# Performance work log

Measured on AMD Instinct MI355X. Metric: run time of the kernel, lower is better.

Reference implementation:

```python
import jax, jax.numpy as jnp
import numpy as np

D_MODEL = 1024
NHEAD = 16
HEAD_DIM = D_MODEL // NHEAD


def setup_inputs() -> dict:
    key = jax.random.key(0)
    ks = jax.random.split(key, 11)
    B, S = 2, 2048
    s = 1.0 / np.sqrt(D_MODEL)
    return {
        "query": jax.random.normal(ks[0], (B, S, D_MODEL), jnp.float32),
        "key": jax.random.normal(ks[1], (B, S, D_MODEL), jnp.float32),
        "value": jax.random.normal(ks[2], (B, S, D_MODEL), jnp.float32),
        "wq_w": jax.random.normal(ks[3], (D_MODEL, D_MODEL), jnp.float32) * s,
        "wq_b": jax.random.normal(ks[4], (D_MODEL,), jnp.float32) * s,
        "wk_w": jax.random.normal(ks[5], (D_MODEL, D_MODEL), jnp.float32) * s,
        "wk_b": jax.random.normal(ks[6], (D_MODEL,), jnp.float32) * s,
        "wv_w": jax.random.normal(ks[7], (D_MODEL, D_MODEL), jnp.float32) * s,
        "wv_b": jax.random.normal(ks[8], (D_MODEL,), jnp.float32) * s,
        "wo_w": jax.random.normal(ks[9], (D_MODEL, D_MODEL), jnp.float32) * s,
        "wo_b": jax.random.normal(ks[10], (D_MODEL,), jnp.float32) * s,
    }


def reference(query, key, value, wq_w, wq_b, wk_w, wk_b, wv_w, wv_b, wo_w, wo_b):
    B, S, _ = query.shape
    # torch Linear: x @ W.T + b
    def proj(x, w, b):
        y = x @ w.T + b
        return y.reshape(B, S, NHEAD, HEAD_DIM).transpose(0, 2, 1, 3)  # [B,H,S,Dh]

    Q = proj(query, wq_w, wq_b)
    K = proj(key, wk_w, wk_b)
    V = proj(value, wv_w, wv_b)

    scale = 1.0 / np.sqrt(HEAD_DIM).astype(np.float32)
    scores = jnp.einsum("bhqd,bhkd->bhqk", Q, K) * scale  # [B,H,S,S]
    causal = jnp.tril(jnp.ones((S, S), dtype=bool))
    scores = jnp.where(causal, scores, -jnp.inf)
    attn = jax.nn.softmax(scores, axis=-1)
    out = jnp.einsum("bhqk,bhkd->bhqd", attn, V)  # [B,H,S,Dh]
    out = out.transpose(0, 2, 1, 3).reshape(B, S, D_MODEL)
    return out @ wo_w.T + wo_b
```

## Files before the change

kernel.cpp:

```cpp
#include <hip/hip_runtime.h>
#include <stdint.h>

#define D_MODEL 1024
#define S_LEN   2048
#define NHEAD   16
#define HEAD_DIM 64
#define BATCH   2
#define M_TOT   (BATCH * S_LEN)
#define Q_SCALE 0.18033688011112042f

using bf16x8 = __attribute__((ext_vector_type(8))) short;
using f32x4  = __attribute__((ext_vector_type(4))) float;

__device__ __forceinline__ unsigned short f2bf(float f) {
  union { float f; unsigned int u; } v; v.f = f;
  unsigned int u = v.u;
  return (unsigned short)((u + 0x7FFFu + ((u >> 16) & 1u)) >> 16);
}
__device__ __forceinline__ unsigned int pkbf(float a, float b) {
#if __has_builtin(__builtin_amdgcn_cvt_pk_bf16_f32)
  auto p = __builtin_amdgcn_cvt_pk_bf16_f32(a, b);
  union { decltype(p) v; unsigned int u; } c; c.v = p;
  return c.u;
#else
  return (unsigned int)f2bf(a) | ((unsigned int)f2bf(b) << 16);
#endif
}
__device__ __forceinline__ bf16x8 cvt8(const float* p) {
  const float4 a = *(const float4*)p;
  const float4 b = *(const float4*)(p + 4);
  union { unsigned int u[4]; bf16x8 v; } r;
  r.u[0] = pkbf(a.x, a.y); r.u[1] = pkbf(a.z, a.w);
  r.u[2] = pkbf(b.x, b.y); r.u[3] = pkbf(b.z, b.w);
  return r.v;
}
__device__ __forceinline__ float fexp2(float x) {
#if __has_builtin(__builtin_amdgcn_exp2f)
  return __builtin_amdgcn_exp2f(x);
#else
  return __expf(x * 0.69314718055994531f);
#endif
}
__device__ __forceinline__ void async16(const unsigned short* g, short* l) {
  __builtin_amdgcn_global_load_lds(
      reinterpret_cast<const __attribute__((address_space(1))) unsigned int*>(
          reinterpret_cast<uintptr_t>(g)),
      reinterpret_cast<__attribute__((address_space(3))) unsigned int*>(
          reinterpret_cast<uintptr_t>(l)),
      16, 0, 0);
}

__device__ __forceinline__ void swap32(unsigned int& x, unsigned int& y) {
#if __has_builtin(__builtin_amdgcn_permlane32_swap)
  auto r = __builtin_amdgcn_permlane32_swap(x, y, false, false);
  x = (unsigned int)r[0]; y = (unsigned int)r[1];
#else
  const int lane = threadIdx.x & 63;
  unsigned int sx = (unsigned int)__shfl_xor((int)x, 32);
  unsigned int sy = (unsigned int)__shfl_xor((int)y, 32);
  unsigned int nx = (lane & 32) ? sy : x;
  unsigned int ny = (lane & 32) ? y : sx;
  x = nx; y = ny;
#endif
}
__device__ __forceinline__ void swap16(unsigned int& x, unsigned int& y) {
#if __has_builtin(__builtin_amdgcn_permlane16_swap)
  auto r = __builtin_amdgcn_permlane16_swap(x, y, false, false);
  x = (unsigned int)r[0]; y = (unsigned int)r[1];
#else
  const int lane = threadIdx.x & 63;
  unsigned int sx = (unsigned int)__shfl_xor((int)x, 16);
  unsigned int sy = (unsigned int)__shfl_xor((int)y, 16);
  unsigned int nx = (lane & 16) ? sy : x;
  unsigned int ny = (lane & 16) ? y : sx;
  x = nx; y = ny;
#endif
}

#define LDK 40

__global__ __launch_bounds__(256)
void cast_all(const float* __restrict__ wq, const float* __restrict__ wk,
              const float* __restrict__ wv, const float* __restrict__ wo,
              const float* __restrict__ q, const float* __restrict__ k,
              const float* __restrict__ v,
              unsigned short* __restrict__ wb,
              unsigned short* __restrict__ qb, unsigned short* __restrict__ kb,
              unsigned short* __restrict__ vb)
{
  const int z = blockIdx.y;
  const float* src;
  unsigned short* d;
  size_t n;
  switch (z) {
    case 0: src = wq; d = wb;                                   n = (size_t)D_MODEL * D_MODEL; break;
    case 1: src = wk; d = wb + (size_t)1 * D_MODEL * D_MODEL;   n = (size_t)D_MODEL * D_MODEL; break;
    case 2: src = wv; d = wb + (size_t)2 * D_MODEL * D_MODEL;   n = (size_t)D_MODEL * D_MODEL; break;
    case 3: src = wo; d = wb + (size_t)3 * D_MODEL * D_MODEL;   n = (size_t)D_MODEL * D_MODEL; break;
    case 4: src = q;  d = qb;                                   n = (size_t)M_TOT * D_MODEL;   break;
    case 5: src = k;  d = kb;                                   n = (size_t)M_TOT * D_MODEL;   break;
    default: src = v; d = vb;                                   n = (size_t)M_TOT * D_MODEL;   break;
  }
  const size_t i = ((size_t)blockIdx.x * 256 + threadIdx.x) * 8;
  if (i < n) *(bf16x8*)(d + i) = cvt8(src + i);
}

__device__ __forceinline__ void gemm_tile_lds(const unsigned short* __restrict__ A,
                                              const unsigned short* __restrict__ W,
                                              int m0, int n0,
                                              short* As, short* Bs,
                                              f32x4 acc[4][4])
{
  const int t    = threadIdx.x;
  const int lane = t & 63;
  const int w    = t >> 6;
  const int quad = lane >> 4;
  const int l16  = lane & 15;
  const int wm   = (w >> 1) * 64;
  const int wn   = (w & 1) * 64;
  const int srow = w * 16 + (lane >> 2);
  const int scol = (lane & 3) * 8;

  for (int mt = 0; mt < 4; ++mt)
    for (int nt = 0; nt < 4; ++nt)
      acc[mt][nt] = f32x4{0.f, 0.f, 0.f, 0.f};

  for (int kt = 0; kt < D_MODEL / 32; ++kt) {
    const int kc = kt * 32 + scol;
    __syncthreads();
    async16(A + (size_t)(m0 + srow)      * D_MODEL + kc, As + srow * 32 + scol);
    async16(A + (size_t)(m0 + 64 + srow) * D_MODEL + kc, As + (64 + srow) * 32 + scol);
    async16(W + (size_t)(n0 + srow)      * D_MODEL + kc, Bs + srow * 32 + scol);
    async16(W + (size_t)(n0 + 64 + srow) * D_MODEL + kc, Bs + (64 + srow) * 32 + scol);
    __syncthreads();

    bf16x8 af[4], bfr[4];
    for (int mt = 0; mt < 4; ++mt)
      af[mt] = *(const bf16x8*)(As + (wm + mt * 16 + l16) * 32 + quad * 8);
    for (int nt = 0; nt < 4; ++nt)
      bfr[nt] = *(const bf16x8*)(Bs + (wn + nt * 16 + l16) * 32 + quad * 8);
    for (int mt = 0; mt < 4; ++mt)
      for (int nt = 0; nt < 4; ++nt)
        acc[mt][nt] = __builtin_amdgcn_mfma_f32_16x16x32_bf16(af[mt], bfr[nt], acc[mt][nt], 0, 0, 0);
  }
}

__device__ __forceinline__ void gemm_tile_f32(const float* __restrict__ A,
                                              const unsigned short* __restrict__ W,
                                              int m0, int n0,
                                              short* As, short* Bs,
                                              f32x4 acc[4][4])
{
  const int t    = threadIdx.x;
  const int lane = t & 63;
  const int w    = t >> 6;
  const int quad = lane >> 4;
  const int l16  = lane & 15;
  const int wm   = (w >> 1) * 64;
  const int wn   = (w & 1) * 64;
  const int srow = t >> 2;
  const int scol = (t & 3) * 8;

  for (int mt = 0; mt < 4; ++mt)
    for (int nt = 0; nt < 4; ++nt)
      acc[mt][nt] = f32x4{0.f, 0.f, 0.f, 0.f};

  for (int kt = 0; kt < D_MODEL / 32; ++kt) {
    const int kc = kt * 32 + scol;
    const bf16x8 a0 = cvt8(A + (size_t)(m0 + srow)      * D_MODEL + kc);
    const bf16x8 a1 = cvt8(A + (size_t)(m0 + srow + 64) * D_MODEL + kc);
    const bf16x8 b0 = *(const bf16x8*)(W + (size_t)(n0 + srow)      * D_MODEL + kc);
    const bf16x8 b1 = *(const bf16x8*)(W + (size_t)(n0 + srow + 64) * D_MODEL + kc);
    __syncthreads();
    *(bf16x8*)(As + (srow)      * LDK + scol) = a0;
    *(bf16x8*)(As + (srow + 64) * LDK + scol) = a1;
    *(bf16x8*)(Bs + (srow)      * LDK + scol) = b0;
    *(bf16x8*)(Bs + (srow + 64) * LDK + scol) = b1;
    __syncthreads();

    bf16x8 af[4], bfr[4];
    for (int mt = 0; mt < 4; ++mt)
      af[mt] = *(const bf16x8*)(As + (wm + mt * 16 + l16) * LDK + quad * 8);
    for (int nt = 0; nt < 4; ++nt)
      bfr[nt] = *(const bf16x8*)(Bs + (wn + nt * 16 + l16) * LDK + quad * 8);
    for (int mt = 0; mt < 4; ++mt)
      for (int nt = 0; nt < 4; ++nt)
        acc[mt][nt] = __builtin_amdgcn_mfma_f32_16x16x32_bf16(af[mt], bfr[nt], acc[mt][nt], 0, 0, 0);
  }
}

__device__ __forceinline__ void qkv_epilogue(int z, int m0, int n0,
                                             const float* __restrict__ bias,
                                             float scale,
                                             unsigned short* __restrict__ dst,
                                             f32x4 acc[4][4])
{
  const int t    = threadIdx.x;
  const int lane = t & 63;
  const int w    = t >> 6;
  const int quad = lane >> 4;
  const int l16  = lane & 15;
  const int wm   = (w >> 1) * 64;
  const int wn   = (w & 1) * 64;

  for (int nt = 0; nt < 4; ++nt) {
    const int n = n0 + wn + nt * 16 + l16;
    const float bb = bias[n];
    const int h = n >> 6, d = n & 63;
    for (int mt = 0; mt < 4; ++mt) {
      for (int r = 0; r < 4; ++r) {
        const int m = m0 + wm + mt * 16 + quad * 4 + r;
        const int b = m >> 11, s = m & 2047;
        const unsigned short val = f2bf((acc[mt][nt][r] + bb) * scale);
        if (z < 2)
          dst[((size_t)((b * NHEAD + h) * S_LEN + s)) * HEAD_DIM + d] = val;
        else
          dst[((size_t)((b * NHEAD + h) * HEAD_DIM + d)) * S_LEN + s] = val;
      }
    }
  }
}

__global__ __launch_bounds__(256)
void qkv_fast(const unsigned short* __restrict__ qb,
              const unsigned short* __restrict__ kb,
              const unsigned short* __restrict__ vb,
              const unsigned short* __restrict__ wqb,
              const unsigned short* __restrict__ wkb,
              const unsigned short* __restrict__ wvb,
              const float* __restrict__ bq, const float* __restrict__ bk,
              const float* __restrict__ bv,
              unsigned short* __restrict__ Qh, unsigned short* __restrict__ Kh,
              unsigned short* __restrict__ VhT)
{
  __shared__ __attribute__((aligned(16))) short As[128 * 32];
  __shared__ __attribute__((aligned(16))) short Bs[128 * 32];
  const int z = blockIdx.z;
  const unsigned short* A    = (z == 0) ? qb  : (z == 1) ? kb  : vb;
  const unsigned short* W    = (z == 0) ? wqb : (z == 1) ? wkb : wvb;
  const float*          bias = (z == 0) ? bq  : (z == 1) ? bk  : bv;
  unsigned short*       dst  = (z == 0) ? Qh  : (z == 1) ? Kh  : VhT;
  const float           scale = (z == 0) ? Q_SCALE : 1.0f;

  const int m0 = blockIdx.x * 128, n0 = blockIdx.y * 128;
  f32x4 acc[4][4];
  gemm_tile_lds(A, W, m0, n0, As, Bs, acc);
  qkv_epilogue(z, m0, n0, bias, scale, dst, acc);
}

__global__ __launch_bounds__(256)
void qkv_slow(const float* __restrict__ query, const float* __restrict__ key,
              const float* __restrict__ value,
              const unsigned short* __restrict__ wqb,
              const unsigned short* __restrict__ wkb,
              const unsigned short* __restrict__ wvb,
              const float* __restrict__ bq, const float* __restrict__ bk,
              const float* __restrict__ bv,
              unsigned short* __restrict__ Qh, unsigned short* __restrict__ Kh,
              unsigned short* __restrict__ VhT)
{
  __shared__ __attribute__((aligned(16))) short As[128 * LDK];
  __shared__ __attribute__((aligned(16))) short Bs[128 * LDK];
  const int z = blockIdx.z;
  const float*          A    = (z == 0) ? query : (z == 1) ? key : value;
  const unsigned short* W    = (z == 0) ? wqb   : (z == 1) ? wkb : wvb;
  const float*          bias = (z == 0) ? bq    : (z == 1) ? bk  : bv;
  unsigned short*       dst  = (z == 0) ? Qh    : (z == 1) ? Kh  : VhT;
  const float           scale = (z == 0) ? Q_SCALE : 1.0f;

  const int m0 = blockIdx.x * 128, n0 = blockIdx.y * 128;
  f32x4 acc[4][4];
  gemm_tile_f32(A, W, m0, n0, As, Bs, acc);
  qkv_epilogue(z, m0, n0, bias, scale, dst, acc);
}

__global__ __launch_bounds__(256)
void out_proj(const unsigned short* __restrict__ Oh,
              const unsigned short* __restrict__ wob,
              const float* __restrict__ bo,
              float* __restrict__ dst)
{
  __shared__ __attribute__((aligned(16))) short As[128 * 32];
  __shared__ __attribute__((aligned(16))) short Bs[128 * 32];
  const int m0 = blockIdx.x * 128, n0 = blockIdx.y * 128;
  f32x4 acc[4][4];
  gemm_tile_lds(Oh, wob, bo ? m0 : m0, n0, As, Bs, acc);

  const int t    = threadIdx.x;
  const int lane = t & 63;
  const int w    = t >> 6;
  const int quad = lane >> 4;
  const int l16  = lane & 15;
  const int wm   = (w >> 1) * 64;
  const int wn   = (w & 1) * 64;

  for (int nt = 0; nt < 4; ++nt) {
    const int n = n0 + wn + nt * 16 + l16;
    const float bb = bo[n];
    for (int mt = 0; mt < 4; ++mt)
      for (int r = 0; r < 4; ++r) {
        const int m = m0 + wm + mt * 16 + quad * 4 + r;
        dst[(size_t)m * D_MODEL + n] = acc[mt][nt][r] + bb;
      }
  }
}

__global__ __launch_bounds__(256)
void attn_kernel(const unsigned short* __restrict__ Qh,
                 const unsigned short* __restrict__ Kh,
                 const unsigned short* __restrict__ VhT,
                 unsigned short* __restrict__ O)
{
  __shared__ __attribute__((aligned(16))) short Ks[128 * 72];
  __shared__ __attribute__((aligned(16))) short Vts[64 * 136];

  const int bh   = blockIdx.x;
  const int qt   = (int)gridDim.y - 1 - (int)blockIdx.y;
  const int q0   = qt * 64;
  const int b    = bh >> 4;
  const int h    = bh & 15;
  const int t    = threadIdx.x;
  const int w    = t >> 6;
  const int lane = t & 63;
  const int quad = lane >> 4;
  const int l16  = lane & 15;
  const size_t headK = (size_t)bh * S_LEN * HEAD_DIM;
  const size_t headV = (size_t)bh * HEAD_DIM * S_LEN;

  bf16x8 qf[2];
  {
    const size_t qrow = (size_t)bh * S_LEN + (q0 + w * 16 + l16);
    qf[0] = *(const bf16x8*)(Qh + qrow * HEAD_DIM + quad * 8);
    qf[1] = *(const bf16x8*)(Qh + qrow * HEAD_DIM + 32 + quad * 8);
  }
  bf16x8 ones;
  for (int j = 0; j < 8; ++j) ones[j] = (short)0x3F80;

  f32x4 lacc = f32x4{0.f, 0.f, 0.f, 0.f};
  f32x4 oacc[4];
  for (int dt = 0; dt < 4; ++dt) oacc[dt] = f32x4{0.f, 0.f, 0.f, 0.f};

  const int rowbase = q0 + w * 16;
  const int rowmax  = rowbase + 15;
  const int qg      = rowbase + l16;
  const int kr = t >> 3, kc = (t & 7) * 8;
  const int vd = t >> 4, vc = (t & 15) * 8;

  const int nkt = (qt + 2) >> 1;
  for (int kt = 0; kt < nkt; ++kt) {
    const int k0 = kt * 128;
    __syncthreads();
    for (int i = 0; i < 4; ++i) {
      const int rr = kr + i * 32;
      *(bf16x8*)(Ks + rr * 72 + kc) =
          *(const bf16x8*)(Kh + headK + (size_t)(k0 + rr) * HEAD_DIM + kc);
      const int dd = vd + i * 16;
      *(bf16x8*)(Vts + dd * 136 + vc) =
          *(const bf16x8*)(VhT + headV + (size_t)dd * S_LEN + k0 + vc);
    }
    __syncthreads();

    float st[8][4];
#pragma unroll
    for (int nt = 0; nt < 8; ++nt) {
      const int c0 = k0 + nt * 16;
      if (c0 <= rowmax) {
        f32x4 s = f32x4{0.f, 0.f, 0.f, 0.f};
#pragma unroll
        for (int ks = 0; ks < 2; ++ks) {
          const bf16x8 kf = *(const bf16x8*)(Ks + (nt * 16 + l16) * 72 + ks * 32 + quad * 8);
          s = __builtin_amdgcn_mfma_f32_16x16x32_bf16(kf, qf[ks], s, 0, 0, 0);
        }
        if (c0 + 15 <= rowbase) {
#pragma unroll
          for (int r = 0; r < 4; ++r) st[nt][r] = fexp2(s[r]);
        } else {
          const int kgb = c0 + quad * 4;
#pragma unroll
          for (int r = 0; r < 4; ++r)
            st[nt][r] = (kgb + r <= qg) ? fexp2(s[r]) : 0.f;
        }
      } else {
#pragma unroll
        for (int r = 0; r < 4; ++r) st[nt][r] = 0.f;
      }
    }

#pragma unroll
    for (int ks = 0; ks < 4; ++ks) {
      if (k0 + ks * 32 <= rowmax) {
        unsigned int pa = pkbf(st[2 * ks][0],     st[2 * ks][1]);
        unsigned int pb = pkbf(st[2 * ks][2],     st[2 * ks][3]);
        unsigned int pc = pkbf(st[2 * ks + 1][0], st[2 * ks + 1][1]);
        unsigned int pe = pkbf(st[2 * ks + 1][2], st[2 * ks + 1][3]);
        swap32(pa, pc); swap32(pb, pe);
        swap16(pa, pc); swap16(pb, pe);
        union { unsigned int u[4]; bf16x8 v; } pf;
        pf.u[0] = pa; pf.u[1] = pb; pf.u[2] = pc; pf.u[3] = pe;
        lacc = __builtin_amdgcn_mfma_f32_16x16x32_bf16(pf.v, ones, lacc, 0, 0, 0);
#pragma unroll
        for (int dt = 0; dt < 4; ++dt) {
          const bf16x8 vf = *(const bf16x8*)(Vts + (dt * 16 + l16) * 136 + ks * 32 + quad * 8);
          oacc[dt] = __builtin_amdgcn_mfma_f32_16x16x32_bf16(pf.v, vf, oacc[dt], 0, 0, 0);
        }
      }
    }
  }

  for (int dt = 0; dt < 4; ++dt) {
    for (int r = 0; r < 4; ++r) {
      const int rowg = q0 + w * 16 + quad * 4 + r;
      O[(size_t)(b * S_LEN + rowg) * D_MODEL + h * 64 + dt * 16 + l16] =
          f2bf(oacc[dt][r] / lacc[r]);
    }
  }
}

extern "C" void kernel_launch(void* const* d_in, const int* in_sizes, int n_in,
                              void* d_out, int out_size, void* d_ws, size_t ws_size,
                              hipStream_t stream)
{
  (void)in_sizes; (void)n_in; (void)out_size;
  const float* q  = (const float*)d_in[0];
  const float* k  = (const float*)d_in[1];
  const float* v  = (const float*)d_in[2];
  const float* wq = (const float*)d_in[3];
  const float* bq = (const float*)d_in[4];
  const float* wk = (const float*)d_in[5];
  const float* bk = (const float*)d_in[6];
  const float* wv = (const float*)d_in[7];
  const float* bv = (const float*)d_in[8];
  const float* wo = (const float*)d_in[9];
  const float* bo = (const float*)d_in[10];
  float* out = (float*)d_out;

  unsigned short* wb  = (unsigned short*)d_ws;
  unsigned short* wqb = wb;
  unsigned short* wkb = wb + (size_t)1 * D_MODEL * D_MODEL;
  unsigned short* wvb = wb + (size_t)2 * D_MODEL * D_MODEL;
  unsigned short* wob = wb + (size_t)3 * D_MODEL * D_MODEL;
  unsigned short* Kh  = wb + (size_t)4 * D_MODEL * D_MODEL;
  unsigned short* VhT = Kh + (size_t)M_TOT * D_MODEL;
  unsigned short* Oh  = VhT + (size_t)M_TOT * D_MODEL;
  unsigned short* qb  = Oh;
  unsigned short* vb  = Oh + (size_t)M_TOT * D_MODEL;
  unsigned short* Qh  = (unsigned short*)d_out;
  unsigned short* kb  = Qh + (size_t)M_TOT * D_MODEL;

  const bool fast = ws_size >= (size_t)40 * 1024 * 1024;

  dim3 g1(M_TOT / 128, D_MODEL / 128, 3);
  if (fast) {
    dim3 gc((size_t)M_TOT * D_MODEL / (256 * 8), 7, 1);
    cast_all<<<gc, 256, 0, stream>>>(wq, wk, wv, wo, q, k, v, wb, qb, kb, vb);
    qkv_fast<<<g1, 256, 0, stream>>>(qb, kb, vb, wqb, wkb, wvb, bq, bk, bv, Qh, Kh, VhT);
  } else {
    dim3 gc((size_t)D_MODEL * D_MODEL / (256 * 8), 4, 1);
    cast_all<<<gc, 256, 0, stream>>>(wq, wk, wv, wo, q, k, v, wb, qb, kb, vb);
    qkv_slow<<<g1, 256, 0, stream>>>(q, k, v, wqb, wkb, wvb, bq, bk, bv, Qh, Kh, VhT);
  }

  dim3 g2(BATCH * NHEAD, S_LEN / 64, 1);
  attn_kernel<<<g2, 256, 0, stream>>>(Qh, Kh, VhT, Oh);

  dim3 g3(M_TOT / 128, D_MODEL / 128, 1);
  out_proj<<<g3, 256, 0, stream>>>(Oh, wob, bo, out);
}
```

Baseline: 217.8 us.

## Rewrite attention to load K/V fragments directly from global memory, without LDS

The attention kernel drops LDS staging and block-wide barriers. Each wave now owns 32 query rows in a 128-row tile and walks its own key range in 32-key chunks, with register double-buffered global loads of K and V fragments and a separate masked path for the diagonal chunk. The grid is flattened to 512 blocks with an XCD-aware mapping that keeps each head's blocks on one XCD for L2 reuse, and heavy causal tiles are scheduled first. This trades shared-memory reuse for more global and L2 traffic and higher register pressure, but removes synchronisation and gives each wave exactly the work its causal span needs.

```diff
diff --git a/kernel.cpp b/kernel.cpp
--- a/kernel.cpp
+++ b/kernel.cpp
@@ -284,7 +284,7 @@
   __shared__ __attribute__((aligned(16))) short Bs[128 * 32];
   const int m0 = blockIdx.x * 128, n0 = blockIdx.y * 128;
   f32x4 acc[4][4];
-  gemm_tile_lds(Oh, wob, bo ? m0 : m0, n0, As, Bs, acc);
+  gemm_tile_lds(Oh, wob, m0, n0, As, Bs, acc);
 
   const int t    = threadIdx.x;
   const int lane = t & 63;
@@ -305,18 +305,97 @@
   }
 }
 
+struct Frags { bf16x8 ka0, ka1, kb0, kb1, v0, v1, v2, v3; };
+
+__device__ __forceinline__ Frags load_frags(const unsigned short* __restrict__ Kb,
+                                            const unsigned short* __restrict__ Vb,
+                                            int c0, int koff, int voff) {
+  Frags f;
+  const unsigned short* kp = Kb + (size_t)c0 * HEAD_DIM + koff;
+  f.ka0 = *(const bf16x8*)(kp);
+  f.ka1 = *(const bf16x8*)(kp + 32);
+  f.kb0 = *(const bf16x8*)(kp + 16 * HEAD_DIM);
+  f.kb1 = *(const bf16x8*)(kp + 16 * HEAD_DIM + 32);
+  const unsigned short* vp = Vb + voff + c0;
+  f.v0 = *(const bf16x8*)(vp);
+  f.v1 = *(const bf16x8*)(vp + 16 * S_LEN);
+  f.v2 = *(const bf16x8*)(vp + 32 * S_LEN);
+  f.v3 = *(const bf16x8*)(vp + 48 * S_LEN);
+  return f;
+}
+
+template <bool DIAG>
+__device__ __forceinline__ void proc_chunk(const Frags& f, const bf16x8 qf[2][2],
+                                           const bf16x8& ones, int quad, int l16,
+                                           f32x4 lacc[2], f32x4 oacc[2][4]) {
+  f32x4 sA0 = f32x4{0.f, 0.f, 0.f, 0.f};
+  f32x4 sA1 = f32x4{0.f, 0.f, 0.f, 0.f};
+  f32x4 sB0 = f32x4{0.f, 0.f, 0.f, 0.f};
+  f32x4 sB1 = f32x4{0.f, 0.f, 0.f, 0.f};
+  sA0 = __builtin_amdgcn_mfma_f32_16x16x32_bf16(f.ka0, qf[0][0], sA0, 0, 0, 0);
+  sA0 = __builtin_amdgcn_mfma_f32_16x16x32_bf16(f.ka1, qf[0][1], sA0, 0, 0, 0);
+  sA1 = __builtin_amdgcn_mfma_f32_16x16x32_bf16(f.ka0, qf[1][0], sA1, 0, 0, 0);
+  sA1 = __builtin_amdgcn_mfma_f32_16x16x32_bf16(f.ka1, qf[1][1], sA1, 0, 0, 0);
+  if (!DIAG) {
+    sB0 = __builtin_amdgcn_mfma_f32_16x16x32_bf16(f.kb0, qf[0][0], sB0, 0, 0, 0);
+    sB0 = __builtin_amdgcn_mfma_f32_16x16x32_bf16(f.kb1, qf[0][1], sB0, 0, 0, 0);
+  }
+  sB1 = __builtin_amdgcn_mfma_f32_16x16x32_bf16(f.kb0, qf[1][0], sB1, 0, 0, 0);
+  sB1 = __builtin_amdgcn_mfma_f32_16x16x32_bf16(f.kb1, qf[1][1], sB1, 0, 0, 0);
+
+  float stA0[4], stB0[4], stA1[4], stB1[4];
+  const int kl = quad * 4;
+#pragma unroll
+  for (int r = 0; r < 4; ++r) {
+    if (!DIAG) {
+      stA0[r] = fexp2(sA0[r]);
+      stB0[r] = fexp2(sB0[r]);
+      stB1[r] = fexp2(sB1[r]);
+    } else {
+      stA0[r] = (kl + r <= l16) ? fexp2(sA0[r]) : 0.f;
+      stB0[r] = 0.f;
+      stB1[r] = (kl + r <= l16) ? fexp2(sB1[r]) : 0.f;
+    }
+    stA1[r] = fexp2(sA1[r]);
+  }
+
+  unsigned int a0 = pkbf(stA0[0], stA0[1]), b0 = pkbf(stA0[2], stA0[3]);
+  unsigned int c0_ = pkbf(stB0[0], stB0[1]), e0 = pkbf(stB0[2], stB0[3]);
+  swap32(a0, c0_); swap32(b0, e0);
+  swap16(a0, c0_); swap16(b0, e0);
+  union { unsigned int u[4]; bf16x8 v; } p0;
+  p0.u[0] = a0; p0.u[1] = b0; p0.u[2] = c0_; p0.u[3] = e0;
+  unsigned int a1 = pkbf(stA1[0], stA1[1]), b1 = pkbf(stA1[2], stA1[3]);
+  unsigned int c1_ = pkbf(stB1[0], stB1[1]), e1 = pkbf(stB1[2], stB1[3]);
+  swap32(a1, c1_); swap32(b1, e1);
+  swap16(a1, c1_); swap16(b1, e1);
+  union { unsigned int u[4]; bf16x8 v; } p1;
+  p1.u[0] = a1; p1.u[1] = b1; p1.u[2] = c1_; p1.u[3] = e1;
+
+  lacc[0] = __builtin_amdgcn_mfma_f32_16x16x32_bf16(p0.v, ones, lacc[0], 0, 0, 0);
+  lacc[1] = __builtin_amdgcn_mfma_f32_16x16x32_bf16(p1.v, ones, lacc[1], 0, 0, 0);
+  oacc[0][0] = __builtin_amdgcn_mfma_f32_16x16x32_bf16(p0.v, f.v0, oacc[0][0], 0, 0, 0);
+  oacc[1][0] = __builtin_amdgcn_mfma_f32_16x16x32_bf16(p1.v, f.v0, oacc[1][0], 0, 0, 0);
+  oacc[0][1] = __builtin_amdgcn_mfma_f32_16x16x32_bf16(p0.v, f.v1, oacc[0][1], 0, 0, 0);
+  oacc[1][1] = __builtin_amdgcn_mfma_f32_16x16x32_bf16(p1.v, f.v1, oacc[1][1], 0, 0, 0);
+  oacc[0][2] = __builtin_amdgcn_mfma_f32_16x16x32_bf16(p0.v, f.v2, oacc[0][2], 0, 0, 0);
+  oacc[1][2] = __builtin_amdgcn_mfma_f32_16x16x32_bf16(p1.v, f.v2, oacc[1][2], 0, 0, 0);
+  oacc[0][3] = __builtin_amdgcn_mfma_f32_16x16x32_bf16(p0.v, f.v3, oacc[0][3], 0, 0, 0);
+  oacc[1][3] = __builtin_amdgcn_mfma_f32_16x16x32_bf16(p1.v, f.v3, oacc[1][3], 0, 0, 0);
+}
+
 __global__ __launch_bounds__(256)
 void attn_kernel(const unsigned short* __restrict__ Qh,
                  const unsigned short* __restrict__ Kh,
                  const unsigned short* __restrict__ VhT,
                  unsigned short* __restrict__ O)
 {
-  __shared__ __attribute__((aligned(16))) short Ks[128 * 72];
-  __shared__ __attribute__((aligned(16))) short Vts[64 * 136];
-
-  const int bh   = blockIdx.x;
-  const int qt   = (int)gridDim.y - 1 - (int)blockIdx.y;
-  const int q0   = qt * 64;
+  const int orig = blockIdx.x;
+  const int xcd  = orig & 7;
+  const int li   = orig >> 3;
+  const int bh   = xcd * 4 + (li & 3);
+  const int qt   = 15 - (li >> 2);
+  const int q0   = qt * 128;
   const int b    = bh >> 4;
   const int h    = bh & 15;
   const int t    = threadIdx.x;
@@ -324,96 +403,60 @@
   const int lane = t & 63;
   const int quad = lane >> 4;
   const int l16  = lane & 15;
-  const size_t headK = (size_t)bh * S_LEN * HEAD_DIM;
-  const size_t headV = (size_t)bh * HEAD_DIM * S_LEN;
-
-  bf16x8 qf[2];
-  {
-    const size_t qrow = (size_t)bh * S_LEN + (q0 + w * 16 + l16);
-    qf[0] = *(const bf16x8*)(Qh + qrow * HEAD_DIM + quad * 8);
-    qf[1] = *(const bf16x8*)(Qh + qrow * HEAD_DIM + 32 + quad * 8);
+  const int rowbase = q0 + w * 32;
+
+  const unsigned short* Kb = Kh + (size_t)bh * S_LEN * HEAD_DIM;
+  const unsigned short* Vb = VhT + (size_t)bh * HEAD_DIM * S_LEN;
+  const int koff = l16 * HEAD_DIM + quad * 8;
+  const int voff = l16 * S_LEN + quad * 8;
+
+  bf16x8 qf[2][2];
+#pragma unroll
+  for (int mt = 0; mt < 2; ++mt) {
+    const size_t qrow = (size_t)bh * S_LEN + rowbase + mt * 16 + l16;
+    qf[mt][0] = *(const bf16x8*)(Qh + qrow * HEAD_DIM + quad * 8);
+    qf[mt][1] = *(const bf16x8*)(Qh + qrow * HEAD_DIM + 32 + quad * 8);
   }
   bf16x8 ones;
+#pragma unroll
   for (int j = 0; j < 8; ++j) ones[j] = (short)0x3F80;
 
-  f32x4 lacc = f32x4{0.f, 0.f, 0.f, 0.f};
-  f32x4 oacc[4];
-  for (int dt = 0; dt < 4; ++dt) oacc[dt] = f32x4{0.f, 0.f, 0.f, 0.f};
-
-  const int rowbase = q0 + w * 16;
-  const int rowmax  = rowbase + 15;
-  const int qg      = rowbase + l16;
-  const int kr = t >> 3, kc = (t & 7) * 8;
-  const int vd = t >> 4, vc = (t & 15) * 8;
-
-  const int nkt = (qt + 2) >> 1;
-  for (int kt = 0; kt < nkt; ++kt) {
-    const int k0 = kt * 128;
-    __syncthreads();
-    for (int i = 0; i < 4; ++i) {
-      const int rr = kr + i * 32;
-      *(bf16x8*)(Ks + rr * 72 + kc) =
-          *(const bf16x8*)(Kh + headK + (size_t)(k0 + rr) * HEAD_DIM + kc);
-      const int dd = vd + i * 16;
-      *(bf16x8*)(Vts + dd * 136 + vc) =
-          *(const bf16x8*)(VhT + headV + (size_t)dd * S_LEN + k0 + vc);
-    }
-    __syncthreads();
-
-    float st[8][4];
-#pragma unroll
-    for (int nt = 0; nt < 8; ++nt) {
-      const int c0 = k0 + nt * 16;
-      if (c0 <= rowmax) {
-        f32x4 s = f32x4{0.f, 0.f, 0.f, 0.f};
-#pragma unroll
-        for (int ks = 0; ks < 2; ++ks) {
-          const bf16x8 kf = *(const bf16x8*)(Ks + (nt * 16 + l16) * 72 + ks * 32 + quad * 8);
-          s = __builtin_amdgcn_mfma_f32_16x16x32_bf16(kf, qf[ks], s, 0, 0, 0);
-        }
-        if (c0 + 15 <= rowbase) {
-#pragma unroll
-          for (int r = 0; r < 4; ++r) st[nt][r] = fexp2(s[r]);
-        } else {
-          const int kgb = c0 + quad * 4;
-#pragma unroll
-          for (int r = 0; r < 4; ++r)
-            st[nt][r] = (kgb + r <= qg) ? fexp2(s[r]) : 0.f;
-        }
-      } else {
-#pragma unroll
-        for (int r = 0; r < 4; ++r) st[nt][r] = 0.f;
+  f32x4 lacc[2];
+  f32x4 oacc[2][4];
+  lacc[0] = f32x4{0.f, 0.f, 0.f, 0.f};
+  lacc[1] = f32x4{0.f, 0.f, 0.f, 0.f};
+#pragma unroll
+  for (int mt = 0; mt < 2; ++mt)
+#pragma unroll
+    for (int dt = 0; dt < 4; ++dt) oacc[mt][dt] = f32x4{0.f, 0.f, 0.f, 0.f};
+
+  const int nfull = 4 * qt + w;
+  Frags fA = load_frags(Kb, Vb, 0, koff, voff);
+  int i = 0;
+  for (; i + 2 <= nfull; i += 2) {
+    Frags fB = load_frags(Kb, Vb, (i + 1) * 32, koff, voff);
+    proc_chunk<false>(fA, qf, ones, quad, l16, lacc, oacc);
+    fA = load_frags(Kb, Vb, (i + 2) * 32, koff, voff);
+    proc_chunk<false>(fB, qf, ones, quad, l16, lacc, oacc);
+  }
+  if (i < nfull) {
+    Frags fB = load_frags(Kb, Vb, (i + 1) * 32, koff, voff);
+    proc_chunk<false>(fA, qf, ones, quad, l16, lacc, oacc);
+    proc_chunk<true>(fB, qf, ones, quad, l16, lacc, oacc);
+  } else {
+    proc_chunk<true>(fA, qf, ones, quad, l16, lacc, oacc);
+  }
+
+#pragma unroll
+  for (int mt = 0; mt < 2; ++mt)
+#pragma unroll
+    for (int dt = 0; dt < 4; ++dt)
+#pragma unroll
+      for (int r = 0; r < 4; ++r) {
+        const int rowg = rowbase + mt * 16 + quad * 4 + r;
+        O[(size_t)(b * S_LEN + rowg) * D_MODEL + h * 64 + dt * 16 + l16] =
+            f2bf(oacc[mt][dt][r] / lacc[mt][r]);
       }
-    }
-
-#pragma unroll
-    for (int ks = 0; ks < 4; ++ks) {
-      if (k0 + ks * 32 <= rowmax) {
-        unsigned int pa = pkbf(st[2 * ks][0],     st[2 * ks][1]);
-        unsigned int pb = pkbf(st[2 * ks][2],     st[2 * ks][3]);
-        unsigned int pc = pkbf(st[2 * ks + 1][0], st[2 * ks + 1][1]);
-        unsigned int pe = pkbf(st[2 * ks + 1][2], st[2 * ks + 1][3]);
-        swap32(pa, pc); swap32(pb, pe);
-        swap16(pa, pc); swap16(pb, pe);
-        union { unsigned int u[4]; bf16x8 v; } pf;
-        pf.u[0] = pa; pf.u[1] = pb; pf.u[2] = pc; pf.u[3] = pe;
-        lacc = __builtin_amdgcn_mfma_f32_16x16x32_bf16(pf.v, ones, lacc, 0, 0, 0);
-#pragma unroll
-        for (int dt = 0; dt < 4; ++dt) {
-          const bf16x8 vf = *(const bf16x8*)(Vts + (dt * 16 + l16) * 136 + ks * 32 + quad * 8);
-          oacc[dt] = __builtin_amdgcn_mfma_f32_16x16x32_bf16(pf.v, vf, oacc[dt], 0, 0, 0);
-        }
-      }
-    }
-  }
-
-  for (int dt = 0; dt < 4; ++dt) {
-    for (int r = 0; r < 4; ++r) {
-      const int rowg = q0 + w * 16 + quad * 4 + r;
-      O[(size_t)(b * S_LEN + rowg) * D_MODEL + h * 64 + dt * 16 + l16] =
-          f2bf(oacc[dt][r] / lacc[r]);
-    }
-  }
 }
 
 extern "C" void kernel_launch(void* const* d_in, const int* in_sizes, int n_in,
@@ -460,7 +503,7 @@
     qkv_slow<<<g1, 256, 0, stream>>>(q, k, v, wqb, wkb, wvb, bq, bk, bv, Qh, Kh, VhT);
   }
 
-  dim3 g2(BATCH * NHEAD, S_LEN / 64, 1);
+  dim3 g2(512, 1, 1);
   attn_kernel<<<g2, 256, 0, stream>>>(Qh, Kh, VhT, Oh);
 
   dim3 g3(M_TOT / 128, D_MODEL / 128, 1);
```

Result: slower. 263.2 us (+20.8%).
